# Kernel tuning notes

Measured on AMD Instinct MI355X. Metric: run time of the kernel, lower is better.

Reference implementation:

```python
import jax, jax.numpy as jnp
import numpy as np

D_MODEL = 768
N_HEAD = 12
D_K = D_MODEL // N_HEAD
B, S = 2, 2048


def setup_inputs() -> dict:
    key = jax.random.key(0)
    ks = jax.random.split(key, 13)
    scale = 1.0 / np.sqrt(D_MODEL)
    inp = {
        'q': jax.random.normal(ks[0], (B, S, D_MODEL), jnp.float32),
        'k': jax.random.normal(ks[1], (B, S, D_MODEL), jnp.float32),
        'v': jax.random.normal(ks[2], (B, S, D_MODEL), jnp.float32),
        'Wq': jax.random.normal(ks[3], (D_MODEL, D_MODEL), jnp.float32) * scale,
        'bq': jnp.zeros((D_MODEL,), jnp.float32),
        'Wk': jax.random.normal(ks[4], (D_MODEL, D_MODEL), jnp.float32) * scale,
        'bk': jnp.zeros((D_MODEL,), jnp.float32),
        'Wv': jax.random.normal(ks[5], (D_MODEL, D_MODEL), jnp.float32) * scale,
        'bv': jnp.zeros((D_MODEL,), jnp.float32),
        'Wo': jax.random.normal(ks[6], (D_MODEL, D_MODEL), jnp.float32) * scale,
        'bo': jnp.zeros((D_MODEL,), jnp.float32),
        'mask': jax.random.randint(ks[7], (B, 1, S), 0, 2, jnp.int32),
    }
    return inp


def reference(q, k, v, Wq, bq, Wk, bk, Wv, bv, Wo, bo, mask):
    # project and split heads: [B,S,D] -> [B,H,S,Dk]
    def heads(x, W, b):
        y = x @ W + b
        return y.reshape(B, S, N_HEAD, D_K).transpose(0, 2, 1, 3)

    qh = heads(q, Wq, bq)
    kh = heads(k, Wk, bk)
    vh = heads(v, Wv, bv)
    # full score matrix [B,H,S,S] (intentionally materialized, as in source)
    scores = jnp.einsum('bhqd,bhkd->bhqk', qh, kh) / jnp.sqrt(jnp.float32(D_K))
    m = mask[:, None, :, :]  # [B,1,1,S] broadcast over heads and queries
    scores = jnp.where(m == 0, jnp.float32(-1e9), scores)
    p_attn = jax.nn.softmax(scores, axis=-1)
    # dropout omitted (eval / deterministic reference)
    x = jnp.einsum('bhqk,bhkd->bhqd', p_attn, vh)
    x = x.transpose(0, 2, 1, 3).reshape(B, S, D_MODEL)
    return x @ Wo + bo
```

## Files before the change

kernel.cpp:

```cpp
#include <hip/hip_runtime.h>


#define H_ 12
#define DK_ 64
#define B_DIM 2
#define SEQ 2048
#define DM 768
#define MROWS 4096
#define PER_IN ((size_t)MROWS * DM)

typedef short bf16x8 __attribute__((ext_vector_type(8)));
typedef short bf16x4 __attribute__((ext_vector_type(4)));
typedef float f32x4 __attribute__((ext_vector_type(4)));
typedef float f32x16 __attribute__((ext_vector_type(16)));

__device__ inline unsigned short f2bf(float f) {
    union { float f; unsigned int i; } x; x.f = f;
    unsigned int r = x.i + 0x7fff + ((x.i >> 16) & 1);
    return (unsigned short)(r >> 16);
}

__device__ inline unsigned pack2bf(float lo, float hi) {
#if __has_builtin(__builtin_amdgcn_cvt_pk_bf16_f32)
    auto v = __builtin_amdgcn_cvt_pk_bf16_f32(lo, hi);
    return __builtin_bit_cast(unsigned, v);
#else
    return (unsigned)f2bf(lo) | ((unsigned)f2bf(hi) << 16);
#endif
}

__device__ inline f32x16 mfma32x8(bf16x4 a, bf16x4 b, f32x16 c) {
#if __has_builtin(__builtin_amdgcn_mfma_f32_32x32x8bf16_1k)
    return __builtin_amdgcn_mfma_f32_32x32x8bf16_1k(a, b, c, 0, 0, 0);
#else
    asm("v_mfma_f32_32x32x8_bf16 %0, %1, %2, %0" : "+v"(c) : "v"(a), "v"(b));
    return c;
#endif
}

__device__ inline void gload_lds16(const unsigned short* g, unsigned short* ldsbase,
                                   int lane) {
#if __has_builtin(__builtin_amdgcn_global_load_lds)
    __builtin_amdgcn_global_load_lds(
        (const __attribute__((address_space(1))) unsigned int*)g,
        (__attribute__((address_space(3))) unsigned int*)ldsbase, 16, 0, 0);
#else
    *(uint4*)(ldsbase + 8 * lane) = *(const uint4*)g;
#endif
}

__global__ void cvt3(const float* __restrict__ a, const float* __restrict__ b,
                     const float* __restrict__ c,
                     unsigned short* __restrict__ oa, unsigned short* __restrict__ ob,
                     unsigned short* __restrict__ oc) {
    const float* src = blockIdx.y == 0 ? a : (blockIdx.y == 1 ? b : c);
    unsigned short* dst = blockIdx.y == 0 ? oa : (blockIdx.y == 1 ? ob : oc);
    size_t i = ((size_t)blockIdx.x * 256 + threadIdx.x) * 4;
    float4 f = *(const float4*)(src + i);
    ushort4 u;
    u.x = f2bf(f.x); u.y = f2bf(f.y); u.z = f2bf(f.z); u.w = f2bf(f.w);
    *(ushort4*)(dst + i) = u;
}

__global__ void transpose4(const float* __restrict__ w0, const float* __restrict__ w1,
                           const float* __restrict__ w2, const float* __restrict__ w3,
                           unsigned short* __restrict__ outbase) {
    const float* in = blockIdx.z == 0 ? w0 : (blockIdx.z == 1 ? w1 : (blockIdx.z == 2 ? w2 : w3));
    unsigned short* out = outbase + (size_t)blockIdx.z * DM * DM;
    __shared__ unsigned short t[32][33];
    int x = threadIdx.x, y = threadIdx.y;
    int k0 = blockIdx.x * 32, n0 = blockIdx.y * 32;
#pragma unroll
    for (int i = 0; i < 32; i += 8)
        t[y + i][x] = f2bf(in[(size_t)(k0 + y + i) * DM + n0 + x]);
    __syncthreads();
#pragma unroll
    for (int i = 0; i < 32; i += 8)
        out[(size_t)(n0 + y + i) * DM + k0 + x] = t[x][y + i];
}

__global__ __launch_bounds__(256) void transposeV(const unsigned short* __restrict__ Vn,
                                                  unsigned short* __restrict__ Vt) {
    __shared__ unsigned short Tl[64][72];
    int tid = threadIdx.x;
    int s0 = blockIdx.x * 64, bh = blockIdx.y;
    int row = tid >> 2, cb = (tid & 3) * 16;
    const unsigned short* g = Vn + ((size_t)bh * SEQ + s0 + row) * DK_ + cb;
    uint4 a = *(const uint4*)g;
    uint4 b = *(const uint4*)(g + 8);
    unsigned short v[16];
    *(uint4*)&v[0] = a;
    *(uint4*)&v[8] = b;
#pragma unroll
    for (int j = 0; j < 16; j++)
        Tl[cb + j][row] = v[j];
    __syncthreads();
    uint4 o0 = *(const uint4*)&Tl[row][cb];
    uint4 o1 = *(const uint4*)&Tl[row][cb + 8];
    unsigned short* out = Vt + ((size_t)bh * DK_ + row) * SEQ + s0 + cb;
    *(uint4*)out = o0;
    *(uint4*)(out + 8) = o1;
}

template <int QKV>
__global__ __launch_bounds__(256) void gemm128(
    const unsigned short* __restrict__ A0, const unsigned short* __restrict__ A1,
    const unsigned short* __restrict__ A2, const unsigned short* __restrict__ Wt,
    const float* __restrict__ bias0, const float* __restrict__ bias1,
    const float* __restrict__ bias2,
    void* __restrict__ O0, void* __restrict__ O1, void* __restrict__ O2) {
    __shared__ unsigned short S[2][128][64];
    unsigned short (*Al)[64] = S[0];
    unsigned short (*Bl)[64] = S[1];
    const int K = DM;
    int tid = threadIdx.x;
    int wave = tid >> 6, lane = tid & 63, quad = lane >> 4, l15 = lane & 15;
    int wr = wave >> 1, wc = wave & 1;
    int m0 = blockIdx.x * 128, n0 = blockIdx.y * 128;
    int lrow = lane >> 3, lcol = (lane & 7) * 8;

    int mi = 0, nb0 = n0;
    const unsigned short* A = A0;
    const float* bias = bias0;
    void* O = O0;
    if constexpr (QKV) {
        mi = n0 >= 1536 ? 2 : (n0 >= 768 ? 1 : 0);
        nb0 = n0 - mi * 768;
        A = mi == 0 ? A0 : (mi == 1 ? A1 : A2);
        bias = mi == 0 ? bias0 : (mi == 1 ? bias1 : bias2);
        O = mi == 0 ? O0 : (mi == 1 ? O1 : O2);
    }

    f32x4 acc[4][4];
#pragma unroll
    for (int i = 0; i < 4; i++)
#pragma unroll
        for (int j = 0; j < 4; j++)
#pragma unroll
            for (int r = 0; r < 4; r++) acc[i][j][r] = 0.f;

    const unsigned short* gA = A + (size_t)(m0 + 32 * wave + lrow) * K + lcol;
    const unsigned short* gB = Wt + (size_t)(n0 + 32 * wave + lrow) * K + lcol;

    for (int k0 = 0; k0 < K; k0 += 64) {
        __syncthreads();
#pragma unroll
        for (int c = 0; c < 4; c++) {
            gload_lds16(gA + (size_t)8 * c * K + k0, &Al[32 * wave + 8 * c][0], lane);
            gload_lds16(gB + (size_t)8 * c * K + k0, &Bl[32 * wave + 8 * c][0], lane);
        }
        __syncthreads();
#pragma unroll
        for (int ks = 0; ks < 64; ks += 32) {
            bf16x8 af[4], bfr[4];
#pragma unroll
            for (int i = 0; i < 4; i++)
                af[i] = *(const bf16x8*)&Al[64 * wr + 16 * i + l15][ks + 8 * quad];
#pragma unroll
            for (int j = 0; j < 4; j++)
                bfr[j] = *(const bf16x8*)&Bl[64 * wc + 16 * j + l15][ks + 8 * quad];
#pragma unroll
            for (int i = 0; i < 4; i++)
#pragma unroll
                for (int j = 0; j < 4; j++)
                    acc[i][j] = __builtin_amdgcn_mfma_f32_16x16x32_bf16(af[i], bfr[j], acc[i][j], 0, 0, 0);
        }
    }

    if constexpr (!QKV) {
#pragma unroll
        for (int j = 0; j < 4; j++) {
            int nn = nb0 + 64 * wc + 16 * j + l15;
            float bv = bias[nn];
#pragma unroll
            for (int i = 0; i < 4; i++)
#pragma unroll
                for (int r = 0; r < 4; r++) {
                    int m = m0 + 64 * wr + 16 * i + 4 * quad + r;
                    ((float*)O0)[(size_t)m * DM + nn] = acc[i][j][r] + bv;
                }
        }
    } else {
        __syncthreads();
        unsigned short (*Cl)[128] = (unsigned short(*)[128])S;
#pragma unroll
        for (int j = 0; j < 4; j++) {
            float bv = bias[nb0 + 64 * wc + 16 * j + l15];
#pragma unroll
            for (int i = 0; i < 4; i++)
#pragma unroll
                for (int r = 0; r < 4; r++)
                    Cl[64 * wr + 16 * i + 4 * quad + r][64 * wc + 16 * j + l15] =
                        f2bf(acc[i][j][r] + bv);
        }
        __syncthreads();
        int row = tid >> 1, half = tid & 1;
        int m = m0 + row;
        int b = m >> 11, s = m & 2047;
        int h = (nb0 + 64 * half) >> 6;
        unsigned short* og = (unsigned short*)O + ((size_t)(b * H_ + h) * SEQ + s) * DK_;
        const unsigned short* cr = &Cl[row][64 * half];
#pragma unroll
        for (int c = 0; c < 4; c++)
            *(uint4*)(og + 16 * c) = *(const uint4*)(cr + 16 * c);
#pragma unroll
        for (int c = 0; c < 4; c++)
            *(uint4*)(og + 16 * c + 8) = *(const uint4*)(cr + 16 * c + 8);
    }
}

__global__ __launch_bounds__(256) void attn_fa(const unsigned short* __restrict__ Q,
                                               const unsigned short* __restrict__ Kh,
                                               const unsigned short* __restrict__ Vt,
                                               const int* __restrict__ mask,
                                               unsigned short* __restrict__ ctx) {
    __shared__ __align__(16) unsigned short Ql[64][72];
    __shared__ __align__(16) float mb[SEQ];
    __shared__ __align__(16) unsigned short Kl[64][72];
    __shared__ __align__(16) unsigned short Vl[64][68];
    __shared__ __align__(16) float Op[2][32][32];
    __shared__ __align__(16) float lp[2][32];
    int tid = threadIdx.x;
    int wave = tid >> 6, lane = tid & 63;
    int l31 = lane & 31, hi = lane >> 5;
    int qh = wave & 1, kh = wave >> 1;
    int bh = blockIdx.y, b = bh / H_, h = bh % H_;
    int q0 = blockIdx.x * 64;

    {
        int row = tid >> 2, cb = (tid & 3) * 16;
        const unsigned short* gq = Q + ((size_t)bh * SEQ + q0 + row) * DK_ + cb;
        *(uint4*)&Ql[row][cb]     = *(const uint4*)gq;
        *(uint4*)&Ql[row][cb + 8] = *(const uint4*)(gq + 8);
    }
    {
        const int* mp = mask + (size_t)b * SEQ + tid * 8;
        int4 m0_ = *(const int4*)mp;
        int4 m1_ = *(const int4*)(mp + 4);
        float4 f0, f1;
        f0.x = m0_.x ? 0.f : -1e9f; f0.y = m0_.y ? 0.f : -1e9f;
        f0.z = m0_.z ? 0.f : -1e9f; f0.w = m0_.w ? 0.f : -1e9f;
        f1.x = m1_.x ? 0.f : -1e9f; f1.y = m1_.y ? 0.f : -1e9f;
        f1.z = m1_.z ? 0.f : -1e9f; f1.w = m1_.w ? 0.f : -1e9f;
        *(float4*)&mb[tid * 8] = f0;
        *(float4*)&mb[tid * 8 + 4] = f1;
    }
    __syncthreads();

    bf16x8 qf[4];
#pragma unroll
    for (int c = 0; c < 4; c++)
        qf[c] = *(const bf16x8*)&Ql[32 * qh + l31][16 * c + 8 * hi];

    float lrow = 0.f;
    f32x16 o[2][2];
#pragma unroll
    for (int dt = 0; dt < 2; dt++)
#pragma unroll
        for (int p = 0; p < 2; p++)
#pragma unroll
            for (int r = 0; r < 16; r++) o[dt][p][r] = 0.f;

    int krow = tid >> 2, kcb = (tid & 3) * 16;
    const unsigned short* gk = Kh + ((size_t)bh * SEQ + krow) * DK_ + kcb;
    const unsigned short* gv = Vt + ((size_t)bh * DK_ + krow) * SEQ + kcb;

    uint4 kr0 = *(const uint4*)gk, kr1 = *(const uint4*)(gk + 8);
    uint4 vr0 = *(const uint4*)gv, vr1 = *(const uint4*)(gv + 8);

    for (int kt = 0; kt < SEQ / 64; kt++) {
        __syncthreads();
        *(uint4*)&Kl[krow][kcb]     = kr0;
        *(uint4*)&Kl[krow][kcb + 8] = kr1;
        *(uint4*)&Vl[krow][kcb]     = vr0;
        *(uint4*)&Vl[krow][kcb + 8] = vr1;
        __syncthreads();
        if (kt + 1 < SEQ / 64) {
            gk += (size_t)64 * DK_;
            gv += 64;
            kr0 = *(const uint4*)gk; kr1 = *(const uint4*)(gk + 8);
            vr0 = *(const uint4*)gv; vr1 = *(const uint4*)(gv + 8);
        }

        int kbase = 64 * kt + 32 * kh;
        f32x16 sT;
#pragma unroll
        for (int c = 0; c < 4; c++) {
            f32x4 mv = *(const f32x4*)&mb[kbase + 8 * c + 4 * hi];
#pragma unroll
            for (int j = 0; j < 4; j++) sT[4 * c + j] = mv[j];
        }
#pragma unroll
        for (int c = 0; c < 4; c++) {
            bf16x8 kf = *(const bf16x8*)&Kl[32 * kh + l31][16 * c + 8 * hi];
            sT = __builtin_amdgcn_mfma_f32_32x32x16_bf16(kf, qf[c], sT, 0, 0, 0);
        }

        bf16x4 pfrag[4];
#pragma unroll
        for (int c = 0; c < 4; c++) {
            float p0 = __expf(sT[4 * c + 0] * 0.125f);
            float p1 = __expf(sT[4 * c + 1] * 0.125f);
            float p2 = __expf(sT[4 * c + 2] * 0.125f);
            float p3 = __expf(sT[4 * c + 3] * 0.125f);
            lrow += (p0 + p1) + (p2 + p3);
            union { unsigned u[2]; bf16x4 v; } pk;
            pk.u[0] = pack2bf(p0, p1);
            pk.u[1] = pack2bf(p2, p3);
            pfrag[c] = pk.v;
        }

#pragma unroll
        for (int dt = 0; dt < 2; dt++)
#pragma unroll
            for (int c = 0; c < 4; c++) {
                bf16x4 vf = *(const bf16x4*)&Vl[32 * dt + l31][32 * kh + 8 * c + 4 * hi];
                o[dt][c & 1] = mfma32x8(pfrag[c], vf, o[dt][c & 1]);
            }
    }

    lrow += __shfl_xor(lrow, 32);
    float inv = 0.f;
#pragma unroll
    for (int dt = 0; dt < 2; dt++) {
        if (kh == 1) {
#pragma unroll
            for (int r = 0; r < 16; r++) {
                int qrl = (r & 3) + 8 * (r >> 2) + 4 * hi;
                Op[qh][qrl][l31] = o[dt][0][r] + o[dt][1][r];
            }
            if (dt == 0 && hi == 0) lp[qh][l31] = lrow;
        }
        __syncthreads();
        if (kh == 0) {
            if (dt == 0) {
                float l = lrow + lp[qh][l31];
                inv = l > 0.f ? 1.f / l : 0.f;
            }
#pragma unroll
            for (int r = 0; r < 16; r++) {
                int qrl = (r & 3) + 8 * (r >> 2) + 4 * hi;
                float invr = __shfl(inv, qrl);
                int qg = q0 + 32 * qh + qrl;
                size_t base = ((size_t)b * SEQ + qg) * DM + h * DK_;
                float v = o[dt][0][r] + o[dt][1][r] + Op[qh][qrl][l31];
                ctx[base + 32 * dt + l31] = f2bf(v * invr);
            }
        }
        __syncthreads();
    }
}

extern "C" void kernel_launch(void* const* d_in, const int* in_sizes, int n_in,
                              void* d_out, int out_size, void* d_ws, size_t ws_size,
                              hipStream_t stream) {
    const float* q  = (const float*)d_in[0];
    const float* k  = (const float*)d_in[1];
    const float* v  = (const float*)d_in[2];
    const float* Wq = (const float*)d_in[3];
    const float* bq = (const float*)d_in[4];
    const float* Wk = (const float*)d_in[5];
    const float* bk = (const float*)d_in[6];
    const float* Wv = (const float*)d_in[7];
    const float* bv = (const float*)d_in[8];
    const float* Wo = (const float*)d_in[9];
    const float* bo = (const float*)d_in[10];
    const int* mask = (const int*)d_in[11];

    unsigned short* ws = (unsigned short*)d_ws;
    unsigned short* qb = ws;
    unsigned short* kb = ws + PER_IN;
    unsigned short* vb = ws + 2 * PER_IN;
    unsigned short* Qh = ws + 3 * PER_IN;
    unsigned short* Kh = ws + 4 * PER_IN;
    unsigned short* Vhn = ws + 5 * PER_IN;
    unsigned short* WtQKV = ws + 6 * PER_IN;
    unsigned short* WtO = WtQKV + (size_t)3 * DM * DM;
    unsigned short* Vt = vb;
    unsigned short* ctx = qb;

    cvt3<<<dim3(PER_IN / 1024, 3), 256, 0, stream>>>(q, k, v, qb, kb, vb);
    transpose4<<<dim3(DM / 32, DM / 32, 4), dim3(32, 8), 0, stream>>>(Wq, Wk, Wv, Wo, WtQKV);

    gemm128<1><<<dim3(MROWS / 128, 3 * DM / 128), 256, 0, stream>>>(
        qb, kb, vb, WtQKV, bq, bk, bv, Qh, Kh, Vhn);

    transposeV<<<dim3(SEQ / 64, B_DIM * H_), 256, 0, stream>>>(Vhn, Vt);

    attn_fa<<<dim3(SEQ / 64, B_DIM * H_), 256, 0, stream>>>(Qh, Kh, Vt, mask, ctx);

    gemm128<0><<<dim3(MROWS / 128, DM / 128), 256, 0, stream>>>(
        ctx, ctx, ctx, WtO, bo, bo, bo, d_out, d_out, d_out);
}
```

Before: 226.2 us.

## Compact unmasked keys before attention and fold softmax scale into Q

A new mask-scan kernel builds a compacted index of unmasked key positions per batch. A gather kernel packs K and transposed V down to only those keys, zero-padding the last tile, so attention iterates over roughly half as many key tiles. The padding's exp(0) contributions are subtracted from the row sum. The 1/sqrt(dk)·log2e scale is folded into the Q projection so the softmax can use a raw exp2. The change adds two launches, uses the output buffer as scratch for the indices, and drops max-subtraction (as before), so fully masked rows behave differently from the reference.

```diff
diff --git a/kernel.cpp b/kernel.cpp
--- a/kernel.cpp
+++ b/kernel.cpp
@@ -8,6 +8,7 @@
 #define DM 768
 #define MROWS 4096
 #define PER_IN ((size_t)MROWS * DM)
+#define QSCALE 0.18033688011112042f
 
 typedef short bf16x8 __attribute__((ext_vector_type(8)));
 typedef short bf16x4 __attribute__((ext_vector_type(4)));
@@ -26,6 +27,14 @@
     return __builtin_bit_cast(unsigned, v);
 #else
     return (unsigned)f2bf(lo) | ((unsigned)f2bf(hi) << 16);
+#endif
+}
+
+__device__ inline float exp2fast(float x) {
+#if __has_builtin(__builtin_amdgcn_exp2f)
+    return __builtin_amdgcn_exp2f(x);
+#else
+    return exp2f(x);
 #endif
 }
 
@@ -79,25 +88,74 @@
         out[(size_t)(n0 + y + i) * DM + k0 + x] = t[x][y + i];
 }
 
-__global__ __launch_bounds__(256) void transposeV(const unsigned short* __restrict__ Vn,
-                                                  unsigned short* __restrict__ Vt) {
+__global__ __launch_bounds__(256) void maskscan(const int* __restrict__ mask,
+                                                int* __restrict__ idx,
+                                                int* __restrict__ nkeys) {
+    __shared__ int wsum[4];
+    int b = blockIdx.x, tid = threadIdx.x;
+    int lane = tid & 63, wave = tid >> 6;
+    const int* mp = mask + (size_t)b * SEQ + tid * 8;
+    int4 a = *(const int4*)mp;
+    int4 c = *(const int4*)(mp + 4);
+    int m[8] = {a.x, a.y, a.z, a.w, c.x, c.y, c.z, c.w};
+    int pre[8], s = 0;
+#pragma unroll
+    for (int e = 0; e < 8; e++) { pre[e] = s; s += (m[e] != 0); }
+    int incl = s;
+#pragma unroll
+    for (int off = 1; off < 64; off <<= 1) {
+        int v = __shfl_up(incl, off);
+        if (lane >= off) incl += v;
+    }
+    int lexcl = incl - s;
+    if (lane == 63) wsum[wave] = incl;
+    __syncthreads();
+    int base = lexcl;
+    for (int w = 0; w < wave; w++) base += wsum[w];
+#pragma unroll
+    for (int e = 0; e < 8; e++)
+        if (m[e]) idx[b * SEQ + base + pre[e]] = tid * 8 + e;
+    if (tid == 0) nkeys[b] = wsum[0] + wsum[1] + wsum[2] + wsum[3];
+}
+
+__global__ __launch_bounds__(256) void gatherKV(const unsigned short* __restrict__ Kh,
+                                                const unsigned short* __restrict__ Vn,
+                                                const int* __restrict__ idx,
+                                                const int* __restrict__ nkeys,
+                                                unsigned short* __restrict__ Kc,
+                                                unsigned short* __restrict__ Vtc) {
     __shared__ unsigned short Tl[64][72];
     int tid = threadIdx.x;
-    int s0 = blockIdx.x * 64, bh = blockIdx.y;
+    int j0 = blockIdx.x * 64, bh = blockIdx.y, b = bh / H_;
+    int n = nkeys[b];
     int row = tid >> 2, cb = (tid & 3) * 16;
-    const unsigned short* g = Vn + ((size_t)bh * SEQ + s0 + row) * DK_ + cb;
-    uint4 a = *(const uint4*)g;
-    uint4 b = *(const uint4*)(g + 8);
+    int j = j0 + row;
+    int src = j < n ? idx[b * SEQ + j] : -1;
     unsigned short v[16];
-    *(uint4*)&v[0] = a;
-    *(uint4*)&v[8] = b;
-#pragma unroll
-    for (int j = 0; j < 16; j++)
-        Tl[cb + j][row] = v[j];
+    unsigned short* ok = Kc + ((size_t)bh * SEQ + j) * DK_ + cb;
+    if (src >= 0) {
+        const unsigned short* gv = Vn + ((size_t)bh * SEQ + src) * DK_ + cb;
+        *(uint4*)&v[0] = *(const uint4*)gv;
+        *(uint4*)&v[8] = *(const uint4*)(gv + 8);
+        const unsigned short* gk = Kh + ((size_t)bh * SEQ + src) * DK_ + cb;
+        uint4 k0 = *(const uint4*)gk;
+        uint4 k1 = *(const uint4*)(gk + 8);
+        *(uint4*)ok = k0;
+        *(uint4*)(ok + 8) = k1;
+    } else {
+        uint4 z = {0u, 0u, 0u, 0u};
+        *(uint4*)&v[0] = z;
+        *(uint4*)&v[8] = z;
+        *(uint4*)ok = z;
+        *(uint4*)(ok + 8) = z;
+    }
+#pragma unroll
+    for (int e = 0; e < 16; e++)
+        Tl[cb + e][row] = v[e];
     __syncthreads();
     uint4 o0 = *(const uint4*)&Tl[row][cb];
     uint4 o1 = *(const uint4*)&Tl[row][cb + 8];
-    unsigned short* out = Vt + ((size_t)bh * DK_ + row) * SEQ + s0 + cb;
+    unsigned short* out = Vtc + ((size_t)bh * DK_ + row) * SEQ + j0 + cb;
     *(uint4*)out = o0;
     *(uint4*)(out + 8) = o1;
 }
@@ -181,6 +239,7 @@
                 }
         }
     } else {
+        float sc = mi == 0 ? QSCALE : 1.0f;
         __syncthreads();
         unsigned short (*Cl)[128] = (unsigned short(*)[128])S;
 #pragma unroll
@@ -191,7 +250,7 @@
 #pragma unroll
                 for (int r = 0; r < 4; r++)
                     Cl[64 * wr + 16 * i + 4 * quad + r][64 * wc + 16 * j + l15] =
-                        f2bf(acc[i][j][r] + bv);
+                        f2bf((acc[i][j][r] + bv) * sc);
         }
         __syncthreads();
         int row = tid >> 1, half = tid & 1;
@@ -210,12 +269,11 @@
 }
 
 __global__ __launch_bounds__(256) void attn_fa(const unsigned short* __restrict__ Q,
-                                               const unsigned short* __restrict__ Kh,
-                                               const unsigned short* __restrict__ Vt,
-                                               const int* __restrict__ mask,
+                                               const unsigned short* __restrict__ Kc,
+                                               const unsigned short* __restrict__ Vtc,
+                                               const int* __restrict__ nkeys,
                                                unsigned short* __restrict__ ctx) {
     __shared__ __align__(16) unsigned short Ql[64][72];
-    __shared__ __align__(16) float mb[SEQ];
     __shared__ __align__(16) unsigned short Kl[64][72];
     __shared__ __align__(16) unsigned short Vl[64][68];
     __shared__ __align__(16) float Op[2][32][32];
@@ -227,24 +285,16 @@
     int bh = blockIdx.y, b = bh / H_, h = bh % H_;
     int q0 = blockIdx.x * 64;
 
+    int n = nkeys[b];
+    int nt = (n + 63) >> 6;
+    float padf = (float)(nt * 64 - n);
+
     {
         int row = tid >> 2, cb = (tid & 3) * 16;
         const unsigned short* gq = Q + ((size_t)bh * SEQ + q0 + row) * DK_ + cb;
         *(uint4*)&Ql[row][cb]     = *(const uint4*)gq;
         *(uint4*)&Ql[row][cb + 8] = *(const uint4*)(gq + 8);
     }
-    {
-        const int* mp = mask + (size_t)b * SEQ + tid * 8;
-        int4 m0_ = *(const int4*)mp;
-        int4 m1_ = *(const int4*)(mp + 4);
-        float4 f0, f1;
-        f0.x = m0_.x ? 0.f : -1e9f; f0.y = m0_.y ? 0.f : -1e9f;
-        f0.z = m0_.z ? 0.f : -1e9f; f0.w = m0_.w ? 0.f : -1e9f;
-        f1.x = m1_.x ? 0.f : -1e9f; f1.y = m1_.y ? 0.f : -1e9f;
-        f1.z = m1_.z ? 0.f : -1e9f; f1.w = m1_.w ? 0.f : -1e9f;
-        *(float4*)&mb[tid * 8] = f0;
-        *(float4*)&mb[tid * 8 + 4] = f1;
-    }
     __syncthreads();
 
     bf16x8 qf[4];
@@ -262,34 +312,29 @@
             for (int r = 0; r < 16; r++) o[dt][p][r] = 0.f;
 
     int krow = tid >> 2, kcb = (tid & 3) * 16;
-    const unsigned short* gk = Kh + ((size_t)bh * SEQ + krow) * DK_ + kcb;
-    const unsigned short* gv = Vt + ((size_t)bh * DK_ + krow) * SEQ + kcb;
+    const unsigned short* gk = Kc + ((size_t)bh * SEQ + krow) * DK_ + kcb;
+    const unsigned short* gv = Vtc + ((size_t)bh * DK_ + krow) * SEQ + kcb;
 
     uint4 kr0 = *(const uint4*)gk, kr1 = *(const uint4*)(gk + 8);
     uint4 vr0 = *(const uint4*)gv, vr1 = *(const uint4*)(gv + 8);
 
-    for (int kt = 0; kt < SEQ / 64; kt++) {
+    for (int kt = 0; kt < nt; kt++) {
         __syncthreads();
         *(uint4*)&Kl[krow][kcb]     = kr0;
         *(uint4*)&Kl[krow][kcb + 8] = kr1;
         *(uint4*)&Vl[krow][kcb]     = vr0;
         *(uint4*)&Vl[krow][kcb + 8] = vr1;
         __syncthreads();
-        if (kt + 1 < SEQ / 64) {
+        if (kt + 1 < nt) {
             gk += (size_t)64 * DK_;
             gv += 64;
             kr0 = *(const uint4*)gk; kr1 = *(const uint4*)(gk + 8);
             vr0 = *(const uint4*)gv; vr1 = *(const uint4*)(gv + 8);
         }
 
-        int kbase = 64 * kt + 32 * kh;
         f32x16 sT;
 #pragma unroll
-        for (int c = 0; c < 4; c++) {
-            f32x4 mv = *(const f32x4*)&mb[kbase + 8 * c + 4 * hi];
-#pragma unroll
-            for (int j = 0; j < 4; j++) sT[4 * c + j] = mv[j];
-        }
+        for (int r = 0; r < 16; r++) sT[r] = 0.f;
 #pragma unroll
         for (int c = 0; c < 4; c++) {
             bf16x8 kf = *(const bf16x8*)&Kl[32 * kh + l31][16 * c + 8 * hi];
@@ -299,10 +344,10 @@
         bf16x4 pfrag[4];
 #pragma unroll
         for (int c = 0; c < 4; c++) {
-            float p0 = __expf(sT[4 * c + 0] * 0.125f);
-            float p1 = __expf(sT[4 * c + 1] * 0.125f);
-            float p2 = __expf(sT[4 * c + 2] * 0.125f);
-            float p3 = __expf(sT[4 * c + 3] * 0.125f);
+            float p0 = exp2fast(sT[4 * c + 0]);
+            float p1 = exp2fast(sT[4 * c + 1]);
+            float p2 = exp2fast(sT[4 * c + 2]);
+            float p3 = exp2fast(sT[4 * c + 3]);
             lrow += (p0 + p1) + (p2 + p3);
             union { unsigned u[2]; bf16x4 v; } pk;
             pk.u[0] = pack2bf(p0, p1);
@@ -334,7 +379,7 @@
         __syncthreads();
         if (kh == 0) {
             if (dt == 0) {
-                float l = lrow + lp[qh][l31];
+                float l = lrow + lp[qh][l31] - padf;
                 inv = l > 0.f ? 1.f / l : 0.f;
             }
 #pragma unroll
@@ -376,8 +421,11 @@
     unsigned short* Vhn = ws + 5 * PER_IN;
     unsigned short* WtQKV = ws + 6 * PER_IN;
     unsigned short* WtO = WtQKV + (size_t)3 * DM * DM;
-    unsigned short* Vt = vb;
+    unsigned short* Kc = kb;
+    unsigned short* Vtc = vb;
     unsigned short* ctx = qb;
+    int* idx = (int*)d_out;
+    int* nk = idx + B_DIM * SEQ;
 
     cvt3<<<dim3(PER_IN / 1024, 3), 256, 0, stream>>>(q, k, v, qb, kb, vb);
     transpose4<<<dim3(DM / 32, DM / 32, 4), dim3(32, 8), 0, stream>>>(Wq, Wk, Wv, Wo, WtQKV);
@@ -385,9 +433,10 @@
     gemm128<1><<<dim3(MROWS / 128, 3 * DM / 128), 256, 0, stream>>>(
         qb, kb, vb, WtQKV, bq, bk, bv, Qh, Kh, Vhn);
 
-    transposeV<<<dim3(SEQ / 64, B_DIM * H_), 256, 0, stream>>>(Vhn, Vt);
-
-    attn_fa<<<dim3(SEQ / 64, B_DIM * H_), 256, 0, stream>>>(Qh, Kh, Vt, mask, ctx);
+    maskscan<<<dim3(B_DIM), 256, 0, stream>>>(mask, idx, nk);
+    gatherKV<<<dim3(SEQ / 64, B_DIM * H_), 256, 0, stream>>>(Kh, Vhn, idx, nk, Kc, Vtc);
+
+    attn_fa<<<dim3(SEQ / 64, B_DIM * H_), 256, 0, stream>>>(Qh, Kc, Vtc, nk, ctx);
 
     gemm128<0><<<dim3(MROWS / 128, DM / 128), 256, 0, stream>>>(
         ctx, ctx, ctx, WtO, bo, bo, bo, d_out, d_out, d_out);
```

Result: faster. 212.4 us (-6.1%).
